# Optimization experiments

Measured on AMD Instinct MI355X. Metric: run time of the kernel, lower is better.

Reference implementation:

```python
import jax, jax.numpy as jnp
import numpy as np

N, D, K = 65536, 64, 64


def setup_inputs() -> dict:
    key = jax.random.key(0)
    k1, k2, k3, k4, k5 = jax.random.split(key, 5)
    # seed z = (u, x): u ~ U[0,1), x ~ N(0, I_d)
    u = jax.random.uniform(k1, (N, 1), dtype=jnp.float32)
    x = jax.random.normal(k2, (N, D), dtype=jnp.float32)
    z = jnp.concatenate([u, x], axis=-1)  # [N, d+1]
    # parameters, sized/initialized as in GaussianMixture.__init__
    means = 3.0 * jax.random.normal(k3, (K, D), dtype=jnp.float32)
    devsqrt = jnp.eye(D, dtype=jnp.float32) + 0.3 * jax.random.normal(k4, (K, D, D), dtype=jnp.float32)
    devs = jnp.einsum('kij,klj->kil', devsqrt, devsqrt)  # devsqrt @ devsqrt.T per mode
    mix = jax.nn.softmax(jax.random.normal(k5, (K,), dtype=jnp.float32))
    mix_partition = jnp.cumsum(mix)  # [K], monotone boundaries in (0, 1]
    return {"z": z, "means": means, "devs": devs, "mix_partition": mix_partition}


def reference(z, means, devs, mix_partition):
    # split z -> (u, x)
    u = z[..., 0]          # [N]
    x = z[..., 1:]         # [N, d]
    k = means.shape[0]
    # torch.bucketize(u, partition, right=True) == searchsorted side='right'
    idx = jnp.searchsorted(mix_partition, u, side='right')
    idx = jnp.clip(idx, 0, k - 1)  # guard u == 1.0 edge case
    # y = means[i] + devs[i] @ x  (gather fused with batched matvec)
    dy = jnp.einsum('nij,nj->ni', devs[idx], x)
    return means[idx] + dy
```

## Files before the change

### kernel.cpp

```cpp
#include <hip/hip_runtime.h>
#include <hip/hip_bf16.h>
#include <stdint.h>

#define NROWS 65536
#define KMIX 64
#define DD 64
#define ZS 65
#define CHUNK 128
#define NBLK4 ((NROWS / CHUNK) + KMIX)
#define POISON 0xAAAAAAAAu

typedef __bf16 bf16x8 __attribute__((ext_vector_type(8)));
typedef float f32x4 __attribute__((ext_vector_type(4)));

__device__ __forceinline__ unsigned short f2bf(float f) {
  unsigned int x = __float_as_uint(f);
  unsigned int r = (x + 0x7FFFu + ((x >> 16) & 1u)) >> 16;
  return (unsigned short)r;
}

__device__ __forceinline__ void scan_offsets(const uint32_t* __restrict__ cursors,
                                             uint32_t* __restrict__ s_off, int t) {
  uint32_t c = cursors[t] - POISON;
  uint32_t p = ((c + CHUNK - 1) / CHUNK) * CHUNK;
  uint32_t inc = p;
  #pragma unroll
  for (int d = 1; d < 64; d <<= 1) {
    uint32_t v = __shfl_up(inc, d, 64);
    if (t >= d) inc += v;
  }
  s_off[t] = inc - p;
  if (t == 63) s_off[64] = inc;
}

__global__ __launch_bounds__(256) void k_sort(
    const float* __restrict__ z, const float* __restrict__ mix,
    uint32_t* __restrict__ cursors,
    uint32_t* __restrict__ sorted) {
  __shared__ float s_mix[KMIX];
  __shared__ uint32_t s_hist[KMIX];
  __shared__ uint32_t s_base[KMIX];
  const int t = threadIdx.x;
  if (t < KMIX) { s_mix[t] = mix[t]; s_hist[t] = 0u; }
  __syncthreads();
  const int n = blockIdx.x * 256 + t;
  float u = z[(size_t)n * ZS];
  int idx = 0;
  #pragma unroll
  for (int k = 0; k < KMIX; ++k) idx += (s_mix[k] <= u) ? 1 : 0;
  if (idx > KMIX - 1) idx = KMIX - 1;
  uint32_t r = atomicAdd(&s_hist[idx], 1u);
  __syncthreads();
  if (t < KMIX)
    s_base[t] = s_hist[t] ? (atomicAdd(&cursors[t], s_hist[t]) - POISON) : 0u;
  __syncthreads();
  sorted[(size_t)idx * NROWS + s_base[idx] + r] = (uint32_t)n;
}

__global__ __launch_bounds__(512) void k_main(
    const float* __restrict__ z, const float* __restrict__ means,
    const float* __restrict__ devs, const uint32_t* __restrict__ sorted,
    const uint32_t* __restrict__ cursors, float* __restrict__ out) {
  __shared__ uint32_t s_off[KMIX + 1];
  __shared__ uint32_t s_ent[CHUNK];
  __shared__ __align__(16) unsigned short s_devs[DD * 72];
  __shared__ __align__(16) unsigned short s_x[CHUNK * 72];

  const int t = threadIdx.x;
  const int vbase = blockIdx.x * CHUNK;
  const int lane = t & 63, wave = t >> 6;

  if (t < KMIX) scan_offsets(cursors, s_off, t);
  __syncthreads();

  int kb = 0;
  while (kb < KMIX - 1 && s_off[kb + 1] <= (uint32_t)vbase) ++kb;
  const int local = vbase - (int)s_off[kb];
  int nv = (int)(cursors[kb] - POISON) - local;
  if (nv <= 0) return;
  if (nv > CHUNK) nv = CHUNK;
  const uint32_t* seg = sorted + (size_t)kb * NROWS + local;

  if (t < CHUNK) s_ent[t] = (t < nv) ? seg[t] : seg[0];

  {
    const float4* gd = reinterpret_cast<const float4*>(devs + (size_t)kb * DD * DD);
    #pragma unroll
    for (int it = 0; it < 2; ++it) {
      int e = t + it * 512;
      float4 v = gd[e];
      int row = e >> 4, col = (e & 15) * 4;
      ushort4 w = make_ushort4(f2bf(v.x), f2bf(v.y), f2bf(v.z), f2bf(v.w));
      *reinterpret_cast<ushort4*>(&s_devs[row * 72 + col]) = w;
    }
  }
  {
    #pragma unroll
    for (int rr = 0; rr < CHUNK; rr += 8) {
      int rl = rr + wave;
      uint32_t row = (rl < nv) ? seg[rl] : seg[0];
      float xv = z[(size_t)row * ZS + 1 + lane];
      s_x[rl * 72 + lane] = f2bf(xv);
    }
  }
  __syncthreads();

  const int m16 = lane & 15, quad = lane >> 4;

  float mv[4];
  #pragma unroll
  for (int it = 0; it < 4; ++it) mv[it] = means[kb * DD + it * 16 + m16];

  {
    const int g = wave;
    const unsigned short* xr = &s_x[(g * 16 + m16) * 72 + quad * 8];
    bf16x8 a0 = *reinterpret_cast<const bf16x8*>(xr);
    bf16x8 a1 = *reinterpret_cast<const bf16x8*>(xr + 32);

    f32x4 acc[4];
    #pragma unroll
    for (int it = 0; it < 4; ++it) acc[it] = (f32x4){0.f, 0.f, 0.f, 0.f};

    #pragma unroll
    for (int it = 0; it < 4; ++it) {
      const unsigned short* dr = &s_devs[(it * 16 + m16) * 72 + quad * 8];
      bf16x8 b0 = *reinterpret_cast<const bf16x8*>(dr);
      bf16x8 b1 = *reinterpret_cast<const bf16x8*>(dr + 32);
      acc[it] = __builtin_amdgcn_mfma_f32_16x16x32_bf16(a0, b0, acc[it], 0, 0, 0);
      acc[it] = __builtin_amdgcn_mfma_f32_16x16x32_bf16(a1, b1, acc[it], 0, 0, 0);
    }

    #pragma unroll
    for (int reg = 0; reg < 4; ++reg) {
      int rp = g * 16 + quad * 4 + reg;
      if (rp < nv) {
        uint32_t row = s_ent[rp];
        float* orow = out + (size_t)row * DD + m16;
        #pragma unroll
        for (int it = 0; it < 4; ++it) orow[it * 16] = acc[it][reg] + mv[it];
      }
    }
  }
}

extern "C" void kernel_launch(void* const* d_in, const int* in_sizes, int n_in,
                              void* d_out, int out_size, void* d_ws, size_t ws_size,
                              hipStream_t stream) {
  const float* z     = (const float*)d_in[0];
  const float* means = (const float*)d_in[1];
  const float* devs  = (const float*)d_in[2];
  const float* mix   = (const float*)d_in[3];
  float* out = (float*)d_out;

  uint32_t* W = (uint32_t*)d_ws;
  uint32_t* cursors = W;
  uint32_t* sorted  = cursors + KMIX;

  k_sort<<<NROWS / 256, 256, 0, stream>>>(z, mix, cursors, sorted);
  k_main<<<NBLK4, 512, 0, stream>>>(z, means, devs, sorted, cursors, out);
}
```

Baseline: 85.98 us.

## Pre-convert devs to bf16 in sort kernel and load MFMA operands directly

The sort kernel now also converts the covariance matrices to bf16 once into workspace, and each thread handles two rows with half as many blocks. Atomic cursors are padded to separate cache lines. The main kernel finds its mode segment with a ballot/popcount instead of a serial loop, and drops its LDS staging of devs and x, loading MFMA operands straight from global memory. This removes per-block conversion and shared-memory round trips, at the cost of uncoalesced strided global loads for x and fewer, longer sort blocks.

```diff
diff --git a/kernel.cpp b/kernel.cpp
--- a/kernel.cpp
+++ b/kernel.cpp
@@ -1,5 +1,4 @@
 #include <hip/hip_runtime.h>
-#include <hip/hip_bf16.h>
 #include <stdint.h>
 
 #define NROWS 65536
@@ -7,138 +6,141 @@
 #define DD 64
 #define ZS 65
 #define CHUNK 128
-#define NBLK4 ((NROWS / CHUNK) + KMIX)
+#define NBLK ((NROWS / CHUNK) + KMIX)
 #define POISON 0xAAAAAAAAu
+#define CSTR 16
 
 typedef __bf16 bf16x8 __attribute__((ext_vector_type(8)));
 typedef float f32x4 __attribute__((ext_vector_type(4)));
+typedef unsigned short u16x8 __attribute__((ext_vector_type(8)));
 
 __device__ __forceinline__ unsigned short f2bf(float f) {
   unsigned int x = __float_as_uint(f);
-  unsigned int r = (x + 0x7FFFu + ((x >> 16) & 1u)) >> 16;
-  return (unsigned short)r;
-}
-
-__device__ __forceinline__ void scan_offsets(const uint32_t* __restrict__ cursors,
-                                             uint32_t* __restrict__ s_off, int t) {
-  uint32_t c = cursors[t] - POISON;
-  uint32_t p = ((c + CHUNK - 1) / CHUNK) * CHUNK;
-  uint32_t inc = p;
-  #pragma unroll
-  for (int d = 1; d < 64; d <<= 1) {
-    uint32_t v = __shfl_up(inc, d, 64);
-    if (t >= d) inc += v;
-  }
-  s_off[t] = inc - p;
-  if (t == 63) s_off[64] = inc;
+  return (unsigned short)((x + 0x7FFFu + ((x >> 16) & 1u)) >> 16);
 }
 
 __global__ __launch_bounds__(256) void k_sort(
     const float* __restrict__ z, const float* __restrict__ mix,
+    const float* __restrict__ devs,
     uint32_t* __restrict__ cursors,
-    uint32_t* __restrict__ sorted) {
+    uint32_t* __restrict__ sorted,
+    unsigned short* __restrict__ devs_bf) {
   __shared__ float s_mix[KMIX];
   __shared__ uint32_t s_hist[KMIX];
   __shared__ uint32_t s_base[KMIX];
-  const int t = threadIdx.x;
+  const int t = threadIdx.x, b = blockIdx.x;
   if (t < KMIX) { s_mix[t] = mix[t]; s_hist[t] = 0u; }
+
+  {
+    const int k = b >> 1, row = (b & 1) * 32 + (t >> 3), cg = t & 7;
+    const float* src = devs + ((size_t)k * DD + row) * DD + cg * 8;
+    float4 v0 = *reinterpret_cast<const float4*>(src);
+    float4 v1 = *reinterpret_cast<const float4*>(src + 4);
+    u16x8 w;
+    w[0] = f2bf(v0.x); w[1] = f2bf(v0.y); w[2] = f2bf(v0.z); w[3] = f2bf(v0.w);
+    w[4] = f2bf(v1.x); w[5] = f2bf(v1.y); w[6] = f2bf(v1.z); w[7] = f2bf(v1.w);
+    *reinterpret_cast<u16x8*>(devs_bf + ((size_t)k * DD + row) * DD + cg * 8) = w;
+  }
   __syncthreads();
-  const int n = blockIdx.x * 256 + t;
-  float u = z[(size_t)n * ZS];
-  int idx = 0;
+
+  const int n0 = b * 512;
+  int idxv[2]; uint32_t rv[2];
   #pragma unroll
-  for (int k = 0; k < KMIX; ++k) idx += (s_mix[k] <= u) ? 1 : 0;
-  if (idx > KMIX - 1) idx = KMIX - 1;
-  uint32_t r = atomicAdd(&s_hist[idx], 1u);
+  for (int r = 0; r < 2; ++r) {
+    const int n = n0 + r * 256 + t;
+    const float u = z[(size_t)n * ZS];
+    int idx = 0;
+    #pragma unroll
+    for (int k = 0; k < KMIX; ++k) idx += (s_mix[k] <= u) ? 1 : 0;
+    if (idx > KMIX - 1) idx = KMIX - 1;
+    idxv[r] = idx;
+    rv[r] = atomicAdd(&s_hist[idx], 1u);
+  }
   __syncthreads();
   if (t < KMIX)
-    s_base[t] = s_hist[t] ? (atomicAdd(&cursors[t], s_hist[t]) - POISON) : 0u;
+    s_base[t] = s_hist[t] ? (atomicAdd(&cursors[t * CSTR], s_hist[t]) - POISON) : 0u;
   __syncthreads();
-  sorted[(size_t)idx * NROWS + s_base[idx] + r] = (uint32_t)n;
+  #pragma unroll
+  for (int r = 0; r < 2; ++r)
+    sorted[(size_t)idxv[r] * NROWS + s_base[idxv[r]] + rv[r]] = (uint32_t)(n0 + r * 256 + t);
 }
 
 __global__ __launch_bounds__(512) void k_main(
     const float* __restrict__ z, const float* __restrict__ means,
-    const float* __restrict__ devs, const uint32_t* __restrict__ sorted,
-    const uint32_t* __restrict__ cursors, float* __restrict__ out) {
-  __shared__ uint32_t s_off[KMIX + 1];
-  __shared__ uint32_t s_ent[CHUNK];
-  __shared__ __align__(16) unsigned short s_devs[DD * 72];
-  __shared__ __align__(16) unsigned short s_x[CHUNK * 72];
+    const unsigned short* __restrict__ devs_bf,
+    const uint32_t* __restrict__ sorted, const uint32_t* __restrict__ cursors,
+    float* __restrict__ out) {
+  __shared__ int s_map[3];
+  const int t = threadIdx.x;
+  const int lane = t & 63, wave = t >> 6;
+  const int vbase = blockIdx.x * CHUNK;
 
-  const int t = threadIdx.x;
-  const int vbase = blockIdx.x * CHUNK;
-  const int lane = t & 63, wave = t >> 6;
-
-  if (t < KMIX) scan_offsets(cursors, s_off, t);
-  __syncthreads();
-
-  int kb = 0;
-  while (kb < KMIX - 1 && s_off[kb + 1] <= (uint32_t)vbase) ++kb;
-  const int local = vbase - (int)s_off[kb];
-  int nv = (int)(cursors[kb] - POISON) - local;
-  if (nv <= 0) return;
-  if (nv > CHUNK) nv = CHUNK;
-  const uint32_t* seg = sorted + (size_t)kb * NROWS + local;
-
-  if (t < CHUNK) s_ent[t] = (t < nv) ? seg[t] : seg[0];
-
-  {
-    const float4* gd = reinterpret_cast<const float4*>(devs + (size_t)kb * DD * DD);
+  if (wave == 0) {
+    const uint32_t c = cursors[lane * CSTR] - POISON;
+    const uint32_t p = ((c + CHUNK - 1) / CHUNK) * CHUNK;
+    uint32_t inc = p;
     #pragma unroll
-    for (int it = 0; it < 2; ++it) {
-      int e = t + it * 512;
-      float4 v = gd[e];
-      int row = e >> 4, col = (e & 15) * 4;
-      ushort4 w = make_ushort4(f2bf(v.x), f2bf(v.y), f2bf(v.z), f2bf(v.w));
-      *reinterpret_cast<ushort4*>(&s_devs[row * 72 + col]) = w;
+    for (int d = 1; d < 64; d <<= 1) {
+      uint32_t v = __shfl_up(inc, d, 64);
+      if (lane >= d) inc += v;
     }
-  }
-  {
-    #pragma unroll
-    for (int rr = 0; rr < CHUNK; rr += 8) {
-      int rl = rr + wave;
-      uint32_t row = (rl < nv) ? seg[rl] : seg[0];
-      float xv = z[(size_t)row * ZS + 1 + lane];
-      s_x[rl * 72 + lane] = f2bf(xv);
+    const uint32_t off = inc - p;
+    const unsigned long long bal = __ballot(off <= (uint32_t)vbase);
+    const int kb = __popcll(bal) - 1;
+    const int offkb = __shfl((int)off, kb, 64);
+    const int ckb = __shfl((int)c, kb, 64);
+    if (lane == 0) {
+      s_map[0] = kb;
+      s_map[1] = vbase - offkb;
+      s_map[2] = ckb - (vbase - offkb);
     }
   }
   __syncthreads();
+  const int kb = s_map[0], local = s_map[1], nv = s_map[2];
+  if (nv <= 0) return;
 
-  const int m16 = lane & 15, quad = lane >> 4;
+  const uint32_t* __restrict__ seg = sorted + (size_t)kb * NROWS + local;
+  const int m16 = lane & 15, quad = lane >> 4, g = wave;
+
+  bf16x8 b0[4], b1[4];
+  #pragma unroll
+  for (int it = 0; it < 4; ++it) {
+    const unsigned short* dr = devs_bf + ((size_t)kb * DD + it * 16 + m16) * DD + quad * 8;
+    b0[it] = *reinterpret_cast<const bf16x8*>(dr);
+    b1[it] = *reinterpret_cast<const bf16x8*>(dr + 32);
+  }
+
+  const int rm = g * 16 + m16;
+  const uint32_t rowm = (rm < nv) ? seg[rm] : seg[0];
+  const float* xr = z + (size_t)rowm * ZS + 1 + quad * 8;
+  union { u16x8 u; bf16x8 b; } a0, a1;
+  #pragma unroll
+  for (int j = 0; j < 8; ++j) {
+    a0.u[j] = f2bf(xr[j]);
+    a1.u[j] = f2bf(xr[32 + j]);
+  }
 
   float mv[4];
   #pragma unroll
   for (int it = 0; it < 4; ++it) mv[it] = means[kb * DD + it * 16 + m16];
 
-  {
-    const int g = wave;
-    const unsigned short* xr = &s_x[(g * 16 + m16) * 72 + quad * 8];
-    bf16x8 a0 = *reinterpret_cast<const bf16x8*>(xr);
-    bf16x8 a1 = *reinterpret_cast<const bf16x8*>(xr + 32);
+  f32x4 acc[4];
+  #pragma unroll
+  for (int it = 0; it < 4; ++it) acc[it] = (f32x4){0.f, 0.f, 0.f, 0.f};
+  #pragma unroll
+  for (int it = 0; it < 4; ++it) {
+    acc[it] = __builtin_amdgcn_mfma_f32_16x16x32_bf16(a0.b, b0[it], acc[it], 0, 0, 0);
+    acc[it] = __builtin_amdgcn_mfma_f32_16x16x32_bf16(a1.b, b1[it], acc[it], 0, 0, 0);
+  }
 
-    f32x4 acc[4];
-    #pragma unroll
-    for (int it = 0; it < 4; ++it) acc[it] = (f32x4){0.f, 0.f, 0.f, 0.f};
-
-    #pragma unroll
-    for (int it = 0; it < 4; ++it) {
-      const unsigned short* dr = &s_devs[(it * 16 + m16) * 72 + quad * 8];
-      bf16x8 b0 = *reinterpret_cast<const bf16x8*>(dr);
-      bf16x8 b1 = *reinterpret_cast<const bf16x8*>(dr + 32);
-      acc[it] = __builtin_amdgcn_mfma_f32_16x16x32_bf16(a0, b0, acc[it], 0, 0, 0);
-      acc[it] = __builtin_amdgcn_mfma_f32_16x16x32_bf16(a1, b1, acc[it], 0, 0, 0);
-    }
-
-    #pragma unroll
-    for (int reg = 0; reg < 4; ++reg) {
-      int rp = g * 16 + quad * 4 + reg;
-      if (rp < nv) {
-        uint32_t row = s_ent[rp];
-        float* orow = out + (size_t)row * DD + m16;
-        #pragma unroll
-        for (int it = 0; it < 4; ++it) orow[it * 16] = acc[it][reg] + mv[it];
-      }
+  #pragma unroll
+  for (int reg = 0; reg < 4; ++reg) {
+    const int rp = g * 16 + quad * 4 + reg;
+    if (rp < nv) {
+      const uint32_t row = seg[rp];
+      float* orow = out + (size_t)row * DD + m16;
+      #pragma unroll
+      for (int it = 0; it < 4; ++it) orow[it * 16] = acc[it][reg] + mv[it];
     }
   }
 }
@@ -154,8 +156,10 @@
 
   uint32_t* W = (uint32_t*)d_ws;
   uint32_t* cursors = W;
-  uint32_t* sorted  = cursors + KMIX;
+  uint32_t* sorted  = W + KMIX * CSTR;
+  unsigned short* devs_bf =
+      (unsigned short*)(sorted + (size_t)KMIX * NROWS);
 
-  k_sort<<<NROWS / 256, 256, 0, stream>>>(z, mix, cursors, sorted);
-  k_main<<<NBLK4, 512, 0, stream>>>(z, means, devs, sorted, cursors, out);
+  k_sort<<<128, 256, 0, stream>>>(z, mix, devs, cursors, sorted, devs_bf);
+  k_main<<<NBLK, 512, 0, stream>>>(z, means, devs_bf, sorted, cursors, out);
 }
```

After: 86.89 us. No clear change (+1.1%).
